# Kernel optimization log

Measured on AMD Instinct MI355X. Metric: run time of the kernel, lower is better.

Reference implementation:

```python
import jax, jax.numpy as jnp
import numpy as np

NUM_NODES = 512
INPUT_DIM = 64
HID_DIM = 64
K_DIFF = 2          # max_diffusion_step
N_LAYERS = 2
N_SUPPORTS = 1      # filter_type='laplacian'
NUM_MATS = N_SUPPORTS * K_DIFF + 1
CONCAT = INPUT_DIM + HID_DIM  # == HID_DIM + HID_DIM since input_dim == hid_dim


def setup_inputs() -> dict:
    key = jax.random.key(0)
    ks = jax.random.split(key, 8)
    T, B = 48, 32
    inputs = jax.random.normal(ks[0], (T, B, NUM_NODES * INPUT_DIM), dtype=jnp.float32)
    h0 = jnp.zeros((N_LAYERS, B, NUM_NODES * HID_DIM), dtype=jnp.float32)
    supports = jax.random.uniform(ks[1], (N_SUPPORTS, NUM_NODES, NUM_NODES), dtype=jnp.float32) / NUM_NODES
    s = 0.05
    W_gate = jax.random.normal(ks[2], (N_LAYERS, NUM_MATS * CONCAT, 2 * HID_DIM), dtype=jnp.float32) * s
    b_gate = jnp.ones((N_LAYERS, 2 * HID_DIM), dtype=jnp.float32)  # bias_start=1.0
    W_c = jax.random.normal(ks[3], (N_LAYERS, NUM_MATS * CONCAT, HID_DIM), dtype=jnp.float32) * s
    b_c = jnp.zeros((N_LAYERS, HID_DIM), dtype=jnp.float32)
    return {"inputs": inputs, "initial_hidden_state": h0, "supports": supports,
            "W_gate": W_gate, "b_gate": b_gate, "W_c": W_c, "b_c": b_c}


def _gconv(supports, x_flat, h_flat, W, b, out_dim):
    # x_flat: (B, N*d_in), h_flat: (B, N*hid)
    B = x_flat.shape[0]
    xh = jnp.concatenate([x_flat.reshape(B, NUM_NODES, -1),
                          h_flat.reshape(B, NUM_NODES, -1)], axis=-1)  # (B,N,c)
    mats = [xh]
    for i in range(N_SUPPORTS):
        S = supports[i]
        t0, t1 = xh, jnp.einsum('nm,bmc->bnc', S, xh)
        mats.append(t1)
        for _ in range(2, K_DIFF + 1):  # Chebyshev recurrence: x_k = 2 S x_{k-1} - x_{k-2}
            t2 = 2.0 * jnp.einsum('nm,bmc->bnc', S, t1) - t0
            mats.append(t2)
            t0, t1 = t1, t2
    feat = jnp.concatenate(mats, axis=-1)            # (B, N, NUM_MATS*c)
    out = jnp.einsum('bnf,fo->bno', feat, W) + b      # (B, N, out_dim)
    return out


def _dcgru_cell(supports, x, h, Wg, bg, Wc, bc):
    B = x.shape[0]
    gates = jax.nn.sigmoid(_gconv(supports, x, h, Wg, bg, 2 * HID_DIM))  # (B,N,2h)
    r, u = jnp.split(gates, 2, axis=-1)
    rh = (r * h.reshape(B, NUM_NODES, HID_DIM)).reshape(B, NUM_NODES * HID_DIM)
    c = jnp.tanh(_gconv(supports, x, rh, Wc, bc, HID_DIM))               # (B,N,h)
    h3 = h.reshape(B, NUM_NODES, HID_DIM)
    new_h = u * h3 + (1.0 - u) * c
    return new_h.reshape(B, NUM_NODES * HID_DIM)


def reference(inputs, initial_hidden_state, supports, W_gate, b_gate, W_c, b_c):
    current = inputs  # (T, B, N*d)
    final_hidden = []
    for l in range(N_LAYERS):
        def step(h, x, l=l):
            h2 = _dcgru_cell(supports, x, h, W_gate[l], b_gate[l], W_c[l], b_c[l])
            return h2, h2
        hT, outs = jax.lax.scan(step, initial_hidden_state[l], current)
        final_hidden.append(hT)
        current = outs
    return jnp.stack(final_hidden, axis=0), current
```

## Files before the change

kernel.cpp:

```cpp
#include <hip/hip_runtime.h>
#include <math.h>

typedef __bf16 bf16_t;
typedef bf16_t bf16x8 __attribute__((ext_vector_type(8)));
typedef bf16_t bf16x4 __attribute__((ext_vector_type(4)));
typedef float  f32x4  __attribute__((ext_vector_type(4)));
typedef unsigned long long u64_t;

#define NB 32
#define NN 512
#define NH 64
#define NF 384
#define TSTEPS 48

static __device__ __forceinline__ f32x4 mfma16(bf16x8 a, bf16x8 b, f32x4 c){
  return __builtin_amdgcn_mfma_f32_16x16x32_bf16(a, b, c, 0, 0, 0);
}
static __device__ __forceinline__ void gload16(char* lds, const char* g){
  __builtin_amdgcn_global_load_lds((const __attribute__((address_space(1))) void*)g,
                                   (__attribute__((address_space(3))) void*)lds, 16, 0, 0);
}
static __device__ __forceinline__ unsigned pack2(float a, float b){
  bf16_t x = (bf16_t)a, y = (bf16_t)b;
  unsigned short ux = __builtin_bit_cast(unsigned short, x);
  unsigned short uy = __builtin_bit_cast(unsigned short, y);
  return (unsigned)ux | ((unsigned)uy << 16);
}

__global__ __launch_bounds__(256) void k_s2f(const float* __restrict__ S,
                                             float* __restrict__ S2f){
  int idx = blockIdx.x * 256 + threadIdx.x;
  int n = idx >> 9, m = idx & 511;
  float acc = 0.f;
  #pragma unroll 8
  for (int k = 0; k < 512; ++k) acc += S[n * 512 + k] * S[k * 512 + m];
  S2f[idx] = acc;
}

__global__ __launch_bounds__(256) void k_prepS(const float* __restrict__ S,
                                               const float* __restrict__ S2f,
                                               char* __restrict__ dst){
  int id = blockIdx.x * 256 + threadIdx.x;
  int r = id >> 9, k = id & 511;
  float v = (r < 512) ? S[r * 512 + k] : S2f[(r - 512) * 512 + k];
  int rt = r >> 5, rr = r & 31, kt = k >> 6, kk = k & 63;
  size_t off = ((size_t)(rt * 8 + kt)) * 4096 + (size_t)(((rr * 128 + 2 * kk)) ^ ((rr & 7) << 4));
  *(bf16_t*)(dst + off) = (bf16_t)v;
}

__global__ __launch_bounds__(256) void k_prepW(const float* __restrict__ W,
                                               char* __restrict__ dst, int OD){
  int i = blockIdx.x * 256 + threadIdx.x;
  int total = 2 * NF * OD;
  if (i >= total) return;
  int l = i / (NF * OD), rem = i - l * (NF * OD);
  int o = rem / NF, f = rem - o * NF;
  const float* Wl = W + (size_t)l * NF * OD;
  float v;
  if (f < 128)      v = Wl[f * OD + o] - Wl[(256 + f) * OD + o];
  else if (f < 256) v = Wl[f * OD + o];
  else              v = 2.f * Wl[f * OD + o];
  int kt = f >> 6, kk = f & 63;
  size_t off = (size_t)l * (6 * OD * 128) + (size_t)kt * (OD * 128)
             + (size_t)(((o * 128 + 2 * kk)) ^ ((o & 7) << 4));
  *(bf16_t*)(dst + off) = (bf16_t)v;
}

__global__ __launch_bounds__(256) void k_hinit(const float* __restrict__ h0,
                                               float* __restrict__ hNf,
                                               bf16_t* __restrict__ hN){
  size_t i = ((size_t)blockIdx.x * 256 + threadIdx.x) * 8;
  f32x4 a = *(const f32x4*)&h0[i], b = *(const f32x4*)&h0[i + 4];
  *(f32x4*)&hNf[i] = a; *(f32x4*)&hNf[i + 4] = b;
  bf16x8 v;
  #pragma unroll
  for (int q = 0; q < 4; ++q){ v[q] = (bf16_t)a[q]; v[q + 4] = (bf16_t)b[q]; }
  *(bf16x8*)&hN[i] = v;
}

__global__ __launch_bounds__(512, 4) void k_gate(
    const float* __restrict__ inputs, const float* __restrict__ curp, int p,
    const bf16_t* __restrict__ hN, const char* __restrict__ SP,
    const char* __restrict__ WgP, const float* __restrict__ bga,
    bf16_t* __restrict__ rhN, float* __restrict__ uN, bf16_t* __restrict__ Dx)
{
  const int l = blockIdx.y;
  const int t = p - l;
  if (t < 0 || t >= TSTEPS) return;

  __shared__ char smem[81920];
  char* const A0 = smem;            char* const A1 = smem + 16384;
  char* const B0 = smem + 32768;    char* const B1 = smem + 49152;
  char* const FT = smem;
  char* const W0 = smem + 49152;
  char* const W1 = smem + 65536;
  char* const RL = smem + 49152;
  char* const UL = smem + 57344;

  const int L = blockIdx.x;
  const int b  = (L & 7) + ((L >> 6) << 3);
  const int bx = (L >> 3) & 7;
  const int n0 = bx * 64;
  const int tid = threadIdx.x, lane = tid & 63, w = tid >> 6;
  const int fr = lane & 15, ko = (lane >> 4) * 8, ro = (lane >> 4) * 4;
  const int pp = tid >> 4, q4 = tid & 15;
  const int wr = w >> 2, wc = w & 3;
  const int wn = w & 1, wo = w >> 1;

  const float* xall = l ? curp : inputs;
  const float*  xs = xall + ((size_t)t * NB + b) * NN * NH;
  const bf16_t* hbg = hN + ((size_t)(l * NB + b)) * NN * NH;
  const char* const WgPl = WgP + (size_t)l * 98304;
  const float* const bg = bga + l * 128;
  bf16_t* const rh_l = rhN + (size_t)l * NB * NN * NH;
  float*  const u_l  = uN  + (size_t)l * NB * NN * NH;
  bf16_t* const Dx_l = Dx  + (size_t)l * NB * NN * 128;

  f32x4 acc[4][2] = {};
  f32x4 rx0[2], rx1[2]; u64_t rh0[2], rh1[2];
  char* const Abuf[2] = { A0, A1 };
  char* const Bbuf[2] = { B0, B1 };

  auto ldB = [&](int kt, int s){
    int m = kt * 64 + 2 * pp;
    const float* xr = xs + (size_t)m * NH + q4 * 4;
    rx0[s] = *(const f32x4*)xr; rx1[s] = *(const f32x4*)(xr + NH);
    const bf16_t* hr = hbg + (size_t)m * NH + q4 * 4;
    rh0[s] = *(const u64_t*)hr; rh1[s] = *(const u64_t*)(hr + NH);
  };
  auto stB = [&](int s, char* Bb){
    int mby = 4 * pp;
    #pragma unroll
    for (int i = 0; i < 4; ++i){
      int c = q4 * 4 + i;
      *(unsigned*)(Bb + ((c * 128 + mby) ^ (((c >> 2) & 7) << 4))) = pack2(rx0[s][i], rx1[s][i]);
      int c2 = c + 64;
      unsigned uh = (unsigned)((rh0[s] >> (16 * i)) & 0xffffULL)
                  | ((unsigned)((rh1[s] >> (16 * i)) & 0xffffULL) << 16);
      *(unsigned*)(Bb + ((c2 * 128 + mby) ^ (((c2 >> 2) & 7) << 4))) = uh;
    }
  };
  auto gloadA = [&](int kt, char* Ab){
    #pragma unroll
    for (int i = 0; i < 2; ++i){
      int c = w * 2 + i;
      int ti = c >> 2;
      int rt = (ti < 2) ? (bx * 2 + ti) : (16 + bx * 2 + (ti - 2));
      gload16(Ab + c * 1024,
              SP + ((size_t)(rt * 8 + kt)) * 4096 + (c & 3) * 1024 + lane * 16);
    }
  };
  auto gloadW = [&](int j, char* Wb){
    const char* src = WgPl + (size_t)j * 16384 + (w * 64 + lane) * 16;
    gload16(Wb + w * 1024, src);
    gload16(Wb + 8192 + w * 1024, src + 8192);
  };
  auto dmm = [&](const char* Ab, const char* Bb){
    #pragma unroll
    for (int kh = 0; kh < 2; ++kh){
      int kb = 2 * (kh * 32 + ko);
      bf16x8 af[4], bf_[2];
      #pragma unroll
      for (int fm = 0; fm < 4; ++fm){
        int r = wr * 64 + fm * 16 + fr;
        af[fm] = *(const bf16x8*)(Ab + (r >> 5) * 4096 + ((((r & 31) * 128 + kb)) ^ ((r & 7) << 4)));
      }
      #pragma unroll
      for (int fc = 0; fc < 2; ++fc){
        int c = wc * 32 + fc * 16 + fr;
        bf_[fc] = *(const bf16x8*)(Bb + ((c * 128 + kb) ^ (((c >> 2) & 7) << 4)));
      }
      #pragma unroll
      for (int fm = 0; fm < 4; ++fm)
        #pragma unroll
        for (int fc = 0; fc < 2; ++fc)
          acc[fm][fc] = mfma16(af[fm], bf_[fc], acc[fm][fc]);
    }
  };

  gloadA(0, A0);
  ldB(0, 0); stB(0, B0);
  ldB(1, 1);
  __syncthreads();

  #pragma unroll
  for (int kt = 0; kt < 8; ++kt){
    if (kt < 7){
      gloadA(kt + 1, Abuf[(kt + 1) & 1]);
      stB((kt + 1) & 1, Bbuf[(kt + 1) & 1]);
    }
    dmm(Abuf[kt & 1], Bbuf[kt & 1]);
    __syncthreads();
    if (kt < 6) ldB(kt + 2, (kt + 2) & 1);
  }

  gloadW(0, W0); gloadW(1, W1);

  #pragma unroll
  for (int s = 0; s < 2; ++s){
    int i = tid + s * 512;
    int row = i >> 4, c8 = (i & 15) * 8;
    char* fdst = FT + (((row * 768 + 2 * c8)) ^ ((row & 7) << 4));
    if (c8 < 64){
      const float* xr = xs + (size_t)(n0 + row) * NH + c8;
      f32x4 a = *(const f32x4*)xr, bq = *(const f32x4*)(xr + 4);
      bf16x8 v;
      #pragma unroll
      for (int q = 0; q < 4; ++q){ v[q] = (bf16_t)a[q]; v[q + 4] = (bf16_t)bq[q]; }
      *(bf16x8*)fdst = v;
    } else {
      *(bf16x8*)fdst = *(const bf16x8*)(hbg + (size_t)(n0 + row) * NH + (c8 - 64));
    }
  }
  #pragma unroll
  for (int fm = 0; fm < 4; ++fm)
    #pragma unroll
    for (int fc = 0; fc < 2; ++fc)
      #pragma unroll
      for (int q = 0; q < 4; ++q){
        int dr = wr * 64 + fm * 16 + ro + q;
        int nn = dr & 63;
        int col = ((dr < 64) ? 128 : 256) + wc * 32 + fc * 16 + fr;
        *(bf16_t*)(FT + (((nn * 768 + 2 * col)) ^ ((nn & 7) << 4))) = (bf16_t)acc[fm][fc][q];
      }
  __syncthreads();

  #pragma unroll
  for (int s = 0; s < 2; ++s){
    int i = tid + s * 512;
    int row = i >> 4, d8 = (i & 15) * 8;
    int col = (d8 < 64) ? 128 + d8 : 256 + (d8 - 64);
    bf16x8 v = *(const bf16x8*)(FT + (((row * 768 + 2 * col)) ^ ((row & 7) << 4)));
    *(bf16x8*)&Dx_l[((size_t)b * NN + n0 + row) * 128 + d8] = v;
  }

  f32x4 gd[2][2] = {};
  #pragma unroll
  for (int j = 0; j < 6; ++j){
    const char* Wb = (j & 1) ? W1 : W0;
    #pragma unroll
    for (int kh = 0; kh < 2; ++kh){
      int kbf = 2 * (j * 64 + kh * 32 + ko);
      int kbw = 2 * (kh * 32 + ko);
      bf16x8 af[2];
      #pragma unroll
      for (int fm = 0; fm < 2; ++fm){
        int r = wn * 32 + fm * 16 + fr;
        af[fm] = *(const bf16x8*)(FT + ((r * 768 + kbf) ^ ((r & 7) << 4)));
      }
      #pragma unroll
      for (int fo = 0; fo < 2; ++fo){
        int orow = wo * 32 + fo * 16 + fr;
        bf16x8 bw = *(const bf16x8*)(Wb + ((orow * 128 + kbw) ^ ((orow & 7) << 4)));
        #pragma unroll
        for (int fm = 0; fm < 2; ++fm)
          gd[fm][fo] = mfma16(af[fm], bw, gd[fm][fo]);
      }
    }
    __syncthreads();
    if (j < 4) gloadW(j + 2, (j & 1) ? W1 : W0);
  }

  #pragma unroll
  for (int fm = 0; fm < 2; ++fm)
    #pragma unroll
    for (int fo = 0; fo < 2; ++fo){
      int o = wo * 32 + fo * 16 + fr;
      float bias = bg[o];
      #pragma unroll
      for (int q = 0; q < 4; ++q){
        int nn = wn * 32 + fm * 16 + ro + q;
        float g = 1.f / (1.f + __expf(-(gd[fm][fo][q] + bias)));
        if (o < 64){
          float hv = (float)*(const bf16_t*)(FT + (((nn * 768 + 2 * (64 + o))) ^ ((nn & 7) << 4)));
          *(bf16_t*)(RL + ((nn * 128 + 2 * o) ^ ((nn & 7) << 4))) = (bf16_t)(g * hv);
        } else {
          *(float*)(UL + ((nn * 256 + 4 * (o - 64)) ^ ((nn & 7) << 5))) = g;
        }
      }
    }
  __syncthreads();
  {
    int row = tid >> 3, o8 = (tid & 7) * 8;
    bf16x8 v = *(const bf16x8*)(RL + ((row * 128 + 2 * o8) ^ ((row & 7) << 4)));
    *(bf16x8*)&rh_l[((size_t)b * NN + n0 + row) * NH + o8] = v;
    int base = (row * 256 + 4 * o8) ^ ((row & 7) << 5);
    f32x4 u0 = *(const f32x4*)(UL + base);
    f32x4 u1 = *(const f32x4*)(UL + base + 16);
    size_t gi = ((size_t)b * NN + n0 + row) * NH + o8;
    *(f32x4*)&u_l[gi] = u0; *(f32x4*)&u_l[gi + 4] = u1;
  }
}

__global__ __launch_bounds__(512, 4) void k_cand(
    const float* __restrict__ inputs, int p,
    const bf16_t* __restrict__ rhN, const bf16_t* __restrict__ Dx,
    const char* __restrict__ SP, const char* __restrict__ WcP,
    const float* __restrict__ bca, const float* __restrict__ uN,
    float* __restrict__ hNf, bf16_t* __restrict__ hN,
    float* __restrict__ outp)
{
  const int l = blockIdx.y;
  const int t = p - l;
  if (t < 0 || t >= TSTEPS) return;

  __shared__ char smem[65536];
  char* const A0 = smem;            char* const A1 = smem + 16384;
  char* const B0 = smem + 32768;    char* const B1 = smem + 40960;
  char* const FT = smem;
  char* const W0 = smem + 49152;    char* const W1 = smem + 57344;
  char* const CL = smem + 49152;

  const int L = blockIdx.x;
  const int b  = (L & 7) + ((L >> 6) << 3);
  const int bx = (L >> 3) & 7;
  const int n0 = bx * 64;
  const int tid = threadIdx.x, lane = tid & 63, w = tid >> 6;
  const int fr = lane & 15, ko = (lane >> 4) * 8, ro = (lane >> 4) * 4;
  const int pp = tid >> 4, q4 = tid & 15;
  const int wr = w >> 2, wc = w & 3;
  const int wn = w & 1, wo = w >> 1;

  float* const cur = outp + (size_t)2 * NB * NN * NH;
  const float* xall = l ? cur : inputs;
  const float*  xs = xall + ((size_t)t * NB + b) * NN * NH;
  const bf16_t* rbg = rhN + ((size_t)(l * NB + b)) * NN * NH;
  const char* const WcPl = WcP + (size_t)l * 49152;
  const float* const bc = bca + l * 64;
  const bf16_t* const Dx_l = Dx + (size_t)l * NB * NN * 128;
  const float* const u_l = uN + (size_t)l * NB * NN * NH;
  float*  const hNf_l = hNf + (size_t)l * NB * NN * NH;
  bf16_t* const hN_l  = hN  + (size_t)l * NB * NN * NH;
  float* const fin = outp + (size_t)l * NB * NN * NH;

  f32x4 ca[4] = {};
  u64_t rh0[2], rh1[2];
  char* const Abuf[2] = { A0, A1 };
  char* const Bbuf[2] = { B0, B1 };

  auto ldB = [&](int kt, int s){
    int m = kt * 64 + 2 * pp;
    const bf16_t* rr = rbg + (size_t)m * NH + q4 * 4;
    rh0[s] = *(const u64_t*)rr; rh1[s] = *(const u64_t*)(rr + NH);
  };
  auto stB = [&](int s, char* Bb){
    int mby = 4 * pp;
    #pragma unroll
    for (int i = 0; i < 4; ++i){
      int c = q4 * 4 + i;
      unsigned u = (unsigned)((rh0[s] >> (16 * i)) & 0xffffULL)
                 | ((unsigned)((rh1[s] >> (16 * i)) & 0xffffULL) << 16);
      *(unsigned*)(Bb + ((c * 128 + mby) ^ (((c >> 2) & 7) << 4))) = u;
    }
  };
  auto gloadA = [&](int kt, char* Ab){
    #pragma unroll
    for (int i = 0; i < 2; ++i){
      int c = w * 2 + i;
      int ti = c >> 2;
      int rt = (ti < 2) ? (bx * 2 + ti) : (16 + bx * 2 + (ti - 2));
      gload16(Ab + c * 1024,
              SP + ((size_t)(rt * 8 + kt)) * 4096 + (c & 3) * 1024 + lane * 16);
    }
  };
  auto gloadW = [&](int j, char* Wb){
    gload16(Wb + w * 1024, WcPl + (size_t)j * 8192 + (w * 64 + lane) * 16);
  };
  auto cmm = [&](const char* Ab, const char* Bb){
    #pragma unroll
    for (int kh = 0; kh < 2; ++kh){
      int kb = 2 * (kh * 32 + ko);
      int c = wc * 16 + fr;
      bf16x8 bf_ = *(const bf16x8*)(Bb + ((c * 128 + kb) ^ (((c >> 2) & 7) << 4)));
      #pragma unroll
      for (int fm = 0; fm < 4; ++fm){
        int r = wr * 64 + fm * 16 + fr;
        bf16x8 af = *(const bf16x8*)(Ab + (r >> 5) * 4096 + ((((r & 31) * 128 + kb)) ^ ((r & 7) << 4)));
        ca[fm] = mfma16(af, bf_, ca[fm]);
      }
    }
  };

  gloadA(0, A0);
  gloadW(0, W0); gloadW(1, W1);
  ldB(0, 0); stB(0, B0);
  ldB(1, 1);
  __syncthreads();

  #pragma unroll
  for (int kt = 0; kt < 8; ++kt){
    if (kt < 7){
      gloadA(kt + 1, Abuf[(kt + 1) & 1]);
      stB((kt + 1) & 1, Bbuf[(kt + 1) & 1]);
    }
    cmm(Abuf[kt & 1], Bbuf[kt & 1]);
    __syncthreads();
    if (kt < 6) ldB(kt + 2, (kt + 2) & 1);
  }

  #pragma unroll
  for (int s = 0; s < 2; ++s){
    int i = tid + s * 512;
    int row = i >> 4, c8 = (i & 15) * 8;
    char* fdst = FT + (((row * 768 + 2 * c8)) ^ ((row & 7) << 4));
    if (c8 < 64){
      const float* xr = xs + (size_t)(n0 + row) * NH + c8;
      f32x4 a = *(const f32x4*)xr, bq = *(const f32x4*)(xr + 4);
      bf16x8 v;
      #pragma unroll
      for (int q = 0; q < 4; ++q){ v[q] = (bf16_t)a[q]; v[q + 4] = (bf16_t)bq[q]; }
      *(bf16x8*)fdst = v;
    } else {
      *(bf16x8*)fdst = *(const bf16x8*)(rbg + (size_t)(n0 + row) * NH + (c8 - 64));
    }
    int col = (c8 < 64) ? 128 + c8 : 256 + (c8 - 64);
    bf16x8 dv = *(const bf16x8*)&Dx_l[((size_t)b * NN + n0 + row) * 128 + c8];
    *(bf16x8*)(FT + (((row * 768 + 2 * col)) ^ ((row & 7) << 4))) = dv;
  }
  #pragma unroll
  for (int fm = 0; fm < 4; ++fm)
    #pragma unroll
    for (int q = 0; q < 4; ++q){
      int dr = wr * 64 + fm * 16 + ro + q;
      int nn = dr & 63;
      int col = ((dr < 64) ? 192 : 320) + wc * 16 + fr;
      *(bf16_t*)(FT + (((nn * 768 + 2 * col)) ^ ((nn & 7) << 4))) = (bf16_t)ca[fm][q];
    }
  __syncthreads();

  f32x4 cd[2] = {};
  #pragma unroll
  for (int j = 0; j < 6; ++j){
    const char* Wb = (j & 1) ? W1 : W0;
    #pragma unroll
    for (int kh = 0; kh < 2; ++kh){
      int kbf = 2 * (j * 64 + kh * 32 + ko);
      int kbw = 2 * (kh * 32 + ko);
      int orow = wo * 16 + fr;
      bf16x8 bw = *(const bf16x8*)(Wb + ((orow * 128 + kbw) ^ ((orow & 7) << 4)));
      #pragma unroll
      for (int fm = 0; fm < 2; ++fm){
        int r = wn * 32 + fm * 16 + fr;
        bf16x8 af = *(const bf16x8*)(FT + ((r * 768 + kbf) ^ ((r & 7) << 4)));
        cd[fm] = mfma16(af, bw, cd[fm]);
      }
    }
    __syncthreads();
    if (j < 4) gloadW(j + 2, (j & 1) ? W1 : W0);
  }

  #pragma unroll
  for (int fm = 0; fm < 2; ++fm){
    int o = wo * 16 + fr;
    float bias = bc[o];
    #pragma unroll
    for (int q = 0; q < 4; ++q){
      int nn = wn * 32 + fm * 16 + ro + q;
      float e = __expf(2.f * (cd[fm][q] + bias));
      *(float*)(CL + ((nn * 256 + 4 * o) ^ ((nn & 7) << 5))) = (e - 1.f) / (e + 1.f);
    }
  }
  __syncthreads();
  {
    int row = tid >> 3, o8 = (tid & 7) * 8;
    int base = (row * 256 + 4 * o8) ^ ((row & 7) << 5);
    f32x4 c0 = *(const f32x4*)(CL + base);
    f32x4 c1 = *(const f32x4*)(CL + base + 16);
    size_t gi = ((size_t)b * NN + n0 + row) * NH + o8;
    f32x4 u0 = *(const f32x4*)&u_l[gi], u1 = *(const f32x4*)&u_l[gi + 4];
    f32x4 h0v = *(const f32x4*)&hNf_l[gi], h1v = *(const f32x4*)&hNf_l[gi + 4];
    f32x4 n0v, n1v;
    #pragma unroll
    for (int q = 0; q < 4; ++q){
      n0v[q] = u0[q] * h0v[q] + (1.f - u0[q]) * c0[q];
      n1v[q] = u1[q] * h1v[q] + (1.f - u1[q]) * c1[q];
    }
    *(f32x4*)&hNf_l[gi] = n0v; *(f32x4*)&hNf_l[gi + 4] = n1v;
    bf16x8 hb;
    #pragma unroll
    for (int q = 0; q < 4; ++q){ hb[q] = (bf16_t)n0v[q]; hb[q + 4] = (bf16_t)n1v[q]; }
    *(bf16x8*)&hN_l[gi] = hb;
    float* cr = cur + (size_t)t * NB * NN * NH + gi;
    *(f32x4*)cr = n0v; *(f32x4*)(cr + 4) = n1v;
    if (t == TSTEPS - 1){
      *(f32x4*)&fin[gi] = n0v; *(f32x4*)&fin[gi + 4] = n1v;
    }
  }
}

extern "C" void kernel_launch(void* const* d_in, const int* in_sizes, int n_in,
                              void* d_out, int out_size, void* d_ws, size_t ws_size,
                              hipStream_t stream){
  const float* inputs = (const float*)d_in[0];
  const float* h0     = (const float*)d_in[1];
  const float* S      = (const float*)d_in[2];
  const float* W_gate = (const float*)d_in[3];
  const float* b_gate = (const float*)d_in[4];
  const float* W_c    = (const float*)d_in[5];
  const float* b_c    = (const float*)d_in[6];
  float* out = (float*)d_out;
  char* ws = (char*)d_ws;

  char*   SP  =          ws + 0;
  char*   WgP =          ws + 1048576;
  char*   WcP =          ws + 1245184;
  float*  hNf = (float*) (ws + 1343488);
  bf16_t* hN  = (bf16_t*)(ws + 9732096);
  bf16_t* rhN = (bf16_t*)(ws + 13926400);
  float*  uN  = (float*) (ws + 18120704);
  bf16_t* Dx  = (bf16_t*)(ws + 26509312);
  float*  S2f = (float*) (ws + 26509312 + 4194304);

  k_s2f<<<dim3(1024), 256, 0, stream>>>(S, S2f);
  k_prepS<<<dim3(2048), 256, 0, stream>>>(S, S2f, SP);
  k_prepW<<<dim3(384), 256, 0, stream>>>(W_gate, WgP, 128);
  k_prepW<<<dim3(192), 256, 0, stream>>>(W_c, WcP, 64);
  k_hinit<<<dim3(1024), 256, 0, stream>>>(h0, hNf, hN);

  for (int p = 0; p <= TSTEPS; ++p){
    k_gate<<<dim3(256, 2), 512, 0, stream>>>(inputs, out + (size_t)2 * NB * NN * NH,
                                             p, hN, SP, WgP, b_gate, rhN, uN, Dx);
    k_cand<<<dim3(256, 2), 512, 0, stream>>>(inputs, p, rhN, Dx, SP, WcP, b_c, uN,
                                             hNf, hN, out);
  }
}
```

Before: 2.212 ms.

## Emit transposed r*h from gate kernel; candidate kernel reads B operand directly

The gate kernel now also writes r*h in a transposed (channel-major) bf16 layout. The candidate kernel then loads its MFMA B fragments straight from global memory instead of staging them through registers and LDS with a transpose. This removes the B double buffer and its shuffle work. The weight staging also moves to larger two-slice chunks, which halves the W-loop iterations and barriers but grows LDS to 80KB. The cost is an extra global write in k_gate and uncoalesced, uncached-in-LDS global reads inside the inner MMA loop.

```diff
diff --git a/kernel.cpp b/kernel.cpp
--- a/kernel.cpp
+++ b/kernel.cpp
@@ -82,7 +82,8 @@
     const float* __restrict__ inputs, const float* __restrict__ curp, int p,
     const bf16_t* __restrict__ hN, const char* __restrict__ SP,
     const char* __restrict__ WgP, const float* __restrict__ bga,
-    bf16_t* __restrict__ rhN, float* __restrict__ uN, bf16_t* __restrict__ Dx)
+    bf16_t* __restrict__ rhN, bf16_t* __restrict__ rhT,
+    float* __restrict__ uN, bf16_t* __restrict__ Dx)
 {
   const int l = blockIdx.y;
   const int t = p - l;
@@ -112,9 +113,10 @@
   const bf16_t* hbg = hN + ((size_t)(l * NB + b)) * NN * NH;
   const char* const WgPl = WgP + (size_t)l * 98304;
   const float* const bg = bga + l * 128;
-  bf16_t* const rh_l = rhN + (size_t)l * NB * NN * NH;
-  float*  const u_l  = uN  + (size_t)l * NB * NN * NH;
-  bf16_t* const Dx_l = Dx  + (size_t)l * NB * NN * 128;
+  bf16_t* const rh_l  = rhN + (size_t)l * NB * NN * NH;
+  bf16_t* const rhT_l = rhT + (size_t)l * NB * NN * NH;
+  float*  const u_l   = uN  + (size_t)l * NB * NN * NH;
+  bf16_t* const Dx_l  = Dx  + (size_t)l * NB * NN * 128;
 
   f32x4 acc[4][2] = {};
   f32x4 rx0[2], rx1[2]; u64_t rh0[2], rh1[2];
@@ -289,12 +291,21 @@
     f32x4 u1 = *(const f32x4*)(UL + base + 16);
     size_t gi = ((size_t)b * NN + n0 + row) * NH + o8;
     *(f32x4*)&u_l[gi] = u0; *(f32x4*)&u_l[gi + 4] = u1;
+    int o = tid >> 3, n8 = (tid & 7) * 8;
+    bf16x8 tv;
+    #pragma unroll
+    for (int q = 0; q < 8; ++q){
+      int nn = n8 + q;
+      tv[q] = *(const bf16_t*)(RL + ((nn * 128 + 2 * o) ^ ((nn & 7) << 4)));
+    }
+    *(bf16x8*)&rhT_l[((size_t)b * NH + o) * NN + n0 + n8] = tv;
   }
 }
 
 __global__ __launch_bounds__(512, 4) void k_cand(
     const float* __restrict__ inputs, int p,
-    const bf16_t* __restrict__ rhN, const bf16_t* __restrict__ Dx,
+    const bf16_t* __restrict__ rhN, const bf16_t* __restrict__ rhT,
+    const bf16_t* __restrict__ Dx,
     const char* __restrict__ SP, const char* __restrict__ WcP,
     const float* __restrict__ bca, const float* __restrict__ uN,
     float* __restrict__ hNf, bf16_t* __restrict__ hN,
@@ -304,11 +315,10 @@
   const int t = p - l;
   if (t < 0 || t >= TSTEPS) return;
 
-  __shared__ char smem[65536];
+  __shared__ char smem[81920];
   char* const A0 = smem;            char* const A1 = smem + 16384;
-  char* const B0 = smem + 32768;    char* const B1 = smem + 40960;
   char* const FT = smem;
-  char* const W0 = smem + 49152;    char* const W1 = smem + 57344;
+  char* const W0 = smem + 49152;    char* const W1 = smem + 65536;
   char* const CL = smem + 49152;
 
   const int L = blockIdx.x;
@@ -317,14 +327,14 @@
   const int n0 = bx * 64;
   const int tid = threadIdx.x, lane = tid & 63, w = tid >> 6;
   const int fr = lane & 15, ko = (lane >> 4) * 8, ro = (lane >> 4) * 4;
-  const int pp = tid >> 4, q4 = tid & 15;
   const int wr = w >> 2, wc = w & 3;
   const int wn = w & 1, wo = w >> 1;
 
   float* const cur = outp + (size_t)2 * NB * NN * NH;
   const float* xall = l ? cur : inputs;
   const float*  xs = xall + ((size_t)t * NB + b) * NN * NH;
-  const bf16_t* rbg = rhN + ((size_t)(l * NB + b)) * NN * NH;
+  const bf16_t* rbg  = rhN + ((size_t)(l * NB + b)) * NN * NH;
+  const bf16_t* rTg  = rhT + ((size_t)(l * NB + b)) * NN * NH;
   const char* const WcPl = WcP + (size_t)l * 49152;
   const float* const bc = bca + l * 64;
   const bf16_t* const Dx_l = Dx + (size_t)l * NB * NN * 128;
@@ -334,25 +344,8 @@
   float* const fin = outp + (size_t)l * NB * NN * NH;
 
   f32x4 ca[4] = {};
-  u64_t rh0[2], rh1[2];
   char* const Abuf[2] = { A0, A1 };
-  char* const Bbuf[2] = { B0, B1 };
-
-  auto ldB = [&](int kt, int s){
-    int m = kt * 64 + 2 * pp;
-    const bf16_t* rr = rbg + (size_t)m * NH + q4 * 4;
-    rh0[s] = *(const u64_t*)rr; rh1[s] = *(const u64_t*)(rr + NH);
-  };
-  auto stB = [&](int s, char* Bb){
-    int mby = 4 * pp;
-    #pragma unroll
-    for (int i = 0; i < 4; ++i){
-      int c = q4 * 4 + i;
-      unsigned u = (unsigned)((rh0[s] >> (16 * i)) & 0xffffULL)
-                 | ((unsigned)((rh1[s] >> (16 * i)) & 0xffffULL) << 16);
-      *(unsigned*)(Bb + ((c * 128 + mby) ^ (((c >> 2) & 7) << 4))) = u;
-    }
-  };
+
   auto gloadA = [&](int kt, char* Ab){
     #pragma unroll
     for (int i = 0; i < 2; ++i){
@@ -363,15 +356,17 @@
               SP + ((size_t)(rt * 8 + kt)) * 4096 + (c & 3) * 1024 + lane * 16);
     }
   };
-  auto gloadW = [&](int j, char* Wb){
-    gload16(Wb + w * 1024, WcPl + (size_t)j * 8192 + (w * 64 + lane) * 16);
-  };
-  auto cmm = [&](const char* Ab, const char* Bb){
+  auto gloadW2 = [&](int j, char* Wb){
+    const char* src = WcPl + (size_t)(2 * j) * 8192 + (w * 64 + lane) * 16;
+    gload16(Wb + w * 1024, src);
+    gload16(Wb + 8192 + w * 1024, src + 8192);
+  };
+  auto cmm = [&](const char* Ab, int kt){
     #pragma unroll
     for (int kh = 0; kh < 2; ++kh){
       int kb = 2 * (kh * 32 + ko);
       int c = wc * 16 + fr;
-      bf16x8 bf_ = *(const bf16x8*)(Bb + ((c * 128 + kb) ^ (((c >> 2) & 7) << 4)));
+      bf16x8 bf_ = *(const bf16x8*)&rTg[(size_t)c * NN + kt * 64 + kh * 32 + ko];
       #pragma unroll
       for (int fm = 0; fm < 4; ++fm){
         int r = wr * 64 + fm * 16 + fr;
@@ -382,20 +377,14 @@
   };
 
   gloadA(0, A0);
-  gloadW(0, W0); gloadW(1, W1);
-  ldB(0, 0); stB(0, B0);
-  ldB(1, 1);
+  gloadW2(0, W0); gloadW2(1, W1);
   __syncthreads();
 
   #pragma unroll
   for (int kt = 0; kt < 8; ++kt){
-    if (kt < 7){
-      gloadA(kt + 1, Abuf[(kt + 1) & 1]);
-      stB((kt + 1) & 1, Bbuf[(kt + 1) & 1]);
-    }
-    cmm(Abuf[kt & 1], Bbuf[kt & 1]);
+    if (kt < 7) gloadA(kt + 1, Abuf[(kt + 1) & 1]);
+    cmm(Abuf[kt & 1], kt);
     __syncthreads();
-    if (kt < 6) ldB(kt + 2, (kt + 2) & 1);
   }
 
   #pragma unroll
@@ -430,14 +419,15 @@
 
   f32x4 cd[2] = {};
   #pragma unroll
-  for (int j = 0; j < 6; ++j){
+  for (int j = 0; j < 3; ++j){
     const char* Wb = (j & 1) ? W1 : W0;
     #pragma unroll
-    for (int kh = 0; kh < 2; ++kh){
-      int kbf = 2 * (j * 64 + kh * 32 + ko);
-      int kbw = 2 * (kh * 32 + ko);
+    for (int kh = 0; kh < 4; ++kh){
+      int kbf = 2 * (j * 128 + kh * 32 + ko);
+      int sub = (kh >= 2) ? 8192 : 0;
+      int kbw = 2 * ((kh & 1) * 32 + ko);
       int orow = wo * 16 + fr;
-      bf16x8 bw = *(const bf16x8*)(Wb + ((orow * 128 + kbw) ^ ((orow & 7) << 4)));
+      bf16x8 bw = *(const bf16x8*)(Wb + sub + ((orow * 128 + kbw) ^ ((orow & 7) << 4)));
       #pragma unroll
       for (int fm = 0; fm < 2; ++fm){
         int r = wn * 32 + fm * 16 + fr;
@@ -446,7 +436,7 @@
       }
     }
     __syncthreads();
-    if (j < 4) gloadW(j + 2, (j & 1) ? W1 : W0);
+    if (j == 0) gloadW2(2, W0);
   }
 
   #pragma unroll
@@ -509,6 +499,7 @@
   bf16_t* rhN = (bf16_t*)(ws + 13926400);
   float*  uN  = (float*) (ws + 18120704);
   bf16_t* Dx  = (bf16_t*)(ws + 26509312);
+  bf16_t* rhT = (bf16_t*)(ws + 34897920);
   float*  S2f = (float*) (ws + 26509312 + 4194304);
 
   k_s2f<<<dim3(1024), 256, 0, stream>>>(S, S2f);
@@ -519,8 +510,8 @@
 
   for (int p = 0; p <= TSTEPS; ++p){
     k_gate<<<dim3(256, 2), 512, 0, stream>>>(inputs, out + (size_t)2 * NB * NN * NH,
-                                             p, hN, SP, WgP, b_gate, rhN, uN, Dx);
-    k_cand<<<dim3(256, 2), 512, 0, stream>>>(inputs, p, rhN, Dx, SP, WcP, b_c, uN,
-                                             hNf, hN, out);
-  }
-}
+                                             p, hN, SP, WgP, b_gate, rhN, rhT, uN, Dx);
+    k_cand<<<dim3(256, 2), 512, 0, stream>>>(inputs, p, rhN, rhT, Dx, SP, WcP, b_c,
+                                             uN, hNf, hN, out);
+  }
+}
```

Measured after the change: 2.313 ms. 1.05x slower.
